# Optimization experiments

Measured on AMD Instinct MI355X. Metric: run time of the kernel, lower is better.

## Reference

```python
import jax, jax.numpy as jnp
import numpy as np

EMBED_DIM = 2048
NUM_Q_HEADS = 32
NUM_KV_HEADS = 8
HEAD_DIM = EMBED_DIM // NUM_Q_HEADS
N_REP = NUM_Q_HEADS // NUM_KV_HEADS
B, T = 2, 2048


def setup_inputs() -> dict:
    key = jax.random.key(0)
    ks = jax.random.split(key, 10)
    C = EMBED_DIM
    kv_dim = NUM_KV_HEADS * HEAD_DIM
    s = 1.0 / np.sqrt(C)
    return {
        "x": jax.random.normal(ks[0], (B, T, C), dtype=jnp.float32),
        "mask": jnp.tril(jnp.ones((1, 1, T, T), dtype=bool)),
        "Wq": jax.random.normal(ks[1], (C, C), dtype=jnp.float32) * s,
        "bq": jnp.zeros((C,), dtype=jnp.float32),
        "Wk": jax.random.normal(ks[2], (C, kv_dim), dtype=jnp.float32) * s,
        "bk": jnp.zeros((kv_dim,), dtype=jnp.float32),
        "Wv": jax.random.normal(ks[3], (C, kv_dim), dtype=jnp.float32) * s,
        "bv": jnp.zeros((kv_dim,), dtype=jnp.float32),
        "Wo": jax.random.normal(ks[4], (C, C), dtype=jnp.float32) * s,
        "bo": jnp.zeros((C,), dtype=jnp.float32),
    }


def reference(x, mask, Wq, bq, Wk, bk, Wv, bv, Wo, bo):
    b, t, c = x.shape
    # projections
    q = (x @ Wq + bq).reshape(b, t, NUM_Q_HEADS, HEAD_DIM).transpose(0, 2, 1, 3)   # [B,Hq,T,D]
    k = (x @ Wk + bk).reshape(b, t, NUM_KV_HEADS, HEAD_DIM).transpose(0, 2, 1, 3)  # [B,Hkv,T,D]
    v = (x @ Wv + bv).reshape(b, t, NUM_KV_HEADS, HEAD_DIM).transpose(0, 2, 1, 3)
    # repeat KV heads to match query heads (same math as expand+reshape)
    k = jnp.repeat(k, N_REP, axis=1)  # [B,Hq,T,D]
    v = jnp.repeat(v, N_REP, axis=1)
    scores = jnp.einsum("bhqd,bhkd->bhqk", q, k) / np.sqrt(HEAD_DIM)
    scores = jnp.where(mask, scores, -jnp.inf)
    attn = jax.nn.softmax(scores, axis=-1)
    out = jnp.einsum("bhqk,bhkd->bhqd", attn, v)  # [B,Hq,T,D]
    out = out.transpose(0, 2, 1, 3).reshape(b, t, c)
    return out @ Wo + bo
```

## Files before the change

### kernel.cpp

```cpp
#include <hip/hip_runtime.h>
#include <stdint.h>

typedef __attribute__((ext_vector_type(8))) short bf16x8;
typedef __attribute__((ext_vector_type(4))) float f32x4;

#define LOG2E 1.44269504088896f
#define T_SEQ 2048

__device__ __forceinline__ float bf2f(short s) {
    unsigned u = ((unsigned)(unsigned short)s) << 16;
    float f; __builtin_memcpy(&f, &u, 4); return f;
}
__device__ __forceinline__ short f2bf(float f) {
    unsigned u; __builtin_memcpy(&u, &f, 4);
    u = (u + 0x7FFFu + ((u >> 16) & 1u)) >> 16;
    return (short)u;
}
__device__ __forceinline__ short f2bf_trunc(float f) {
    unsigned u; __builtin_memcpy(&u, &f, 4);
    return (short)(u >> 16);
}

#define GLDS(g, l) __builtin_amdgcn_global_load_lds( \
    (const __attribute__((address_space(1))) void*)(g), \
    (__attribute__((address_space(3))) void*)(l), 16, 0, 0)

__global__ void detect_k(const unsigned short* __restrict__ x, int* __restrict__ flag) {
    int lane = threadIdx.x;
    int cnt = 0;
    for (int i = lane; i < 2048; i += 64) {
        int e = (x[i] >> 7) & 0xFF;
        if (e >= 0xC0) cnt++;
    }
    cnt += __shfl_xor(cnt, 1);
    cnt += __shfl_xor(cnt, 2);
    cnt += __shfl_xor(cnt, 4);
    cnt += __shfl_xor(cnt, 8);
    cnt += __shfl_xor(cnt, 16);
    cnt += __shfl_xor(cnt, 32);
    if (lane == 0) { flag[0] = (cnt >= 32) ? 1 : 0; flag[1] = 0; }
}

__global__ __launch_bounds__(256) void convert_k(
    const void* __restrict__ in, short* __restrict__ out, int n,
    const int* __restrict__ flag)
{
    int i = (blockIdx.x * 256 + threadIdx.x) * 8;
    if (i >= n) return;
    bf16x8 v;
    if (*flag) {
        const float* f = (const float*)in + i;
        #pragma unroll
        for (int j = 0; j < 8; ++j) v[j] = f2bf(f[j]);
    } else {
        v = *(const bf16x8*)((const short*)in + i);
    }
    *(bf16x8*)(out + i) = v;
}

__global__ __launch_bounds__(256) void convert4_k(
    const void* __restrict__ b0, const void* __restrict__ b1,
    const void* __restrict__ b2, const void* __restrict__ b3,
    short* __restrict__ o0, short* __restrict__ o1,
    short* __restrict__ o2, short* __restrict__ o3,
    const int* __restrict__ flag)
{
    int i = (blockIdx.x * 256 + threadIdx.x) * 8;
    const void* in; short* out; int off;
    if      (i < 2048) { in = b0; out = o0; off = i; }
    else if (i < 2560) { in = b1; out = o1; off = i - 2048; }
    else if (i < 3072) { in = b2; out = o2; off = i - 2560; }
    else if (i < 5120) { in = b3; out = o3; off = i - 3072; }
    else return;
    bf16x8 v;
    if (*flag) {
        const float* f = (const float*)in + off;
        #pragma unroll
        for (int j = 0; j < 8; ++j) v[j] = f2bf(f[j]);
    } else {
        v = *(const bf16x8*)((const short*)in + off);
    }
    *(bf16x8*)(out + off) = v;
}

__global__ __launch_bounds__(256) void transpose_k(
    const void* __restrict__ in_, short* __restrict__ out,
    int R, int ldi, long ibstride, long obstride, const int* __restrict__ flag)
{
    short* ob = out + (long)blockIdx.z * obstride;
    int c = blockIdx.x * 256 + threadIdx.x;
    int r0 = blockIdx.y * 64;
    int fp32 = *flag;
    if (fp32) {
        const float* ib = (const float*)in_ + (long)blockIdx.z * ibstride;
        for (int rr = 0; rr < 64; rr += 8) {
            bf16x8 v;
            #pragma unroll
            for (int j = 0; j < 8; ++j) v[j] = f2bf(ib[(long)(r0 + rr + j) * ldi + c]);
            *(bf16x8*)(ob + (long)c * R + r0 + rr) = v;
        }
    } else {
        const short* ib = (const short*)in_ + (long)blockIdx.z * ibstride;
        for (int rr = 0; rr < 64; rr += 8) {
            bf16x8 v;
            #pragma unroll
            for (int j = 0; j < 8; ++j) v[j] = ib[(long)(r0 + rr + j) * ldi + c];
            *(bf16x8*)(ob + (long)c * R + r0 + rr) = v;
        }
    }
}

#define BK 32
__global__ __launch_bounds__(256) void gemm_bt(
    const short* __restrict__ A, const short* __restrict__ Bt,
    const short* __restrict__ bias1, int nsplit,
    short* __restrict__ C, short* __restrict__ C2, int n2,
    float* __restrict__ Cf, const int* __restrict__ flag,
    int M, int N, int K, int nbx)
{
    __shared__ short a_lds[128 * BK];
    __shared__ short b_lds[128 * BK];
    const int tid = threadIdx.x;
    const int wave = tid >> 6, lane = tid & 63;
    const int quad = lane >> 4, l16 = lane & 15;

    const int nwg = gridDim.x;
    const int swz = (blockIdx.x & 7) * (nwg >> 3) + (blockIdx.x >> 3);
    const int by = swz / nbx;
    const int bx = swz - by * nbx;
    const int m0 = by * 128, n0 = bx * 128;
    const int wm = (wave >> 1) * 64, wn = (wave & 1) * 64;

    const int c0 = wave * 64 + lane;
    const int c1 = 256 + c0;
    const int row0 = c0 >> 2, kc0 = (c0 & 3) ^ ((row0 >> 1) & 3);
    const int row1 = c1 >> 2, kc1 = (c1 & 3) ^ ((row1 >> 1) & 3);
    const long aoff0 = (long)(m0 + row0) * K + kc0 * 8;
    const long aoff1 = (long)(m0 + row1) * K + kc1 * 8;
    const long boff0 = (long)(n0 + row0) * K + kc0 * 8;
    const long boff1 = (long)(n0 + row1) * K + kc1 * 8;
    short* alp0 = a_lds + (wave * 64) * 8;
    short* alp1 = a_lds + (256 + wave * 64) * 8;
    short* blp0 = b_lds + (wave * 64) * 8;
    short* blp1 = b_lds + (256 + wave * 64) * 8;

    int aro[4], bro[4];
    #pragma unroll
    for (int t = 0; t < 4; ++t) {
        int ra = wm + t * 16 + l16;
        aro[t] = ra * BK + (quad ^ ((ra >> 1) & 3)) * 8;
        int rb = wn + t * 16 + l16;
        bro[t] = rb * BK + (quad ^ ((rb >> 1) & 3)) * 8;
    }

    f32x4 acc[4][4];
    #pragma unroll
    for (int i = 0; i < 4; ++i)
        #pragma unroll
        for (int j = 0; j < 4; ++j)
            acc[i][j] = (f32x4){0.f, 0.f, 0.f, 0.f};

    for (int k0 = 0; k0 < K; k0 += BK) {
        __syncthreads();
        GLDS(A + aoff0 + k0, alp0);
        GLDS(A + aoff1 + k0, alp1);
        GLDS(Bt + boff0 + k0, blp0);
        GLDS(Bt + boff1 + k0, blp1);
        __syncthreads();
        bf16x8 af[4], bfr[4];
        #pragma unroll
        for (int t = 0; t < 4; ++t) af[t] = *(const bf16x8*)(a_lds + aro[t]);
        #pragma unroll
        for (int t = 0; t < 4; ++t) bfr[t] = *(const bf16x8*)(b_lds + bro[t]);
        #pragma unroll
        for (int mt = 0; mt < 4; ++mt)
            #pragma unroll
            for (int nt = 0; nt < 4; ++nt)
                acc[mt][nt] = __builtin_amdgcn_mfma_f32_16x16x32_bf16(
                    af[mt], bfr[nt], acc[mt][nt], 0, 0, 0);
    }

    const int f32o = Cf ? *flag : 0;
    #pragma unroll
    for (int nt = 0; nt < 4; ++nt) {
        int col = n0 + wn + nt * 16 + l16;
        float bb = bf2f(bias1[col < nsplit ? col : 0]);
        #pragma unroll
        for (int mt = 0; mt < 4; ++mt)
            #pragma unroll
            for (int r = 0; r < 4; ++r) {
                int row = m0 + wm + mt * 16 + quad * 4 + r;
                float val = acc[mt][nt][r] + bb;
                if (f32o) {
                    Cf[(long)row * N + col] = val;
                } else if (C2) {
                    if (col < n2) C[(long)row * n2 + col] = f2bf(val);
                    else          C2[(long)row * (N - n2) + (col - n2)] = f2bf(val);
                } else {
                    C[(long)row * N + col] = f2bf(val);
                }
            }
    }
}

#define PLD 68
__global__ __launch_bounds__(256, 4) void attn_k(
    const short* __restrict__ Qf, const short* __restrict__ KVf,
    const short* __restrict__ Vt, short* __restrict__ Attn)
{
    __shared__ short k_lds[64 * PLD];
    __shared__ short vt_lds[64 * PLD];
    __shared__ short p_lds[4 * 32 * PLD];
    const int tid = threadIdx.x;
    const int wave = tid >> 6, lane = tid & 63;
    const int quad = lane >> 4, l16 = lane & 15;

    const int id = blockIdx.x;
    const int bh = id & 63;
    const int w = id >> 6;
    const int QTMAP[16] = {15,13,11,9, 0,2,4,6, 14,12,10,8, 1,3,5,7};
    const int qt = QTMAP[w];
    const int b = bh >> 5, h = bh & 31, hkv = h >> 2;
    const int q0 = qt * 128;
    const int nsteps = 2 * (qt + 1);

    bf16x8 aq[2][2];
    #pragma unroll
    for (int mt = 0; mt < 2; ++mt) {
        const short* qp = Qf + ((long)(b * T_SEQ + q0 + wave * 32 + mt * 16 + l16) * 2048
                                + h * 64 + quad * 8);
        aq[mt][0] = *(const bf16x8*)qp;
        aq[mt][1] = *(const bf16x8*)(qp + 32);
        #pragma unroll
        for (int j = 0; j < 8; ++j) {
            aq[mt][0][j] = f2bf(bf2f(aq[mt][0][j]) * 0.125f);
            aq[mt][1][j] = f2bf(bf2f(aq[mt][1][j]) * 0.125f);
        }
    }

    bf16x8 onesf;
    {
        short o = (l16 == 0) ? (short)0x3F80 : (short)0;
        #pragma unroll
        for (int j = 0; j < 8; ++j) onesf[j] = o;
    }

    f32x4 o_acc[2][4];
    f32x4 l_acc[2];
    #pragma unroll
    for (int mt = 0; mt < 2; ++mt) {
        l_acc[mt] = (f32x4){0.f, 0.f, 0.f, 0.f};
        #pragma unroll
        for (int dt = 0; dt < 4; ++dt) o_acc[mt][dt] = (f32x4){0.f, 0.f, 0.f, 0.f};
    }

    const int cA = tid, cB = 256 + tid;
    const int tA = cA >> 3, chA = cA & 7;
    const int tB = cB >> 3, chB = cB & 7;
    const short* kgA = KVf + ((long)(b * T_SEQ + tA) * 1024 + hkv * 64 + chA * 8);
    const short* kgB = KVf + ((long)(b * T_SEQ + tB) * 1024 + hkv * 64 + chB * 8);
    const short* vgA = Vt + ((long)((b * 8 + hkv) * 64 + tA) * 2048 + chA * 8);
    const short* vgB = Vt + ((long)((b * 8 + hkv) * 64 + tB) * 2048 + chB * 8);

    const int rowq0 = q0 + wave * 32 + quad * 4;
    short* pw = p_lds + (wave * 32 + quad * 4) * PLD + l16;
    const short* pr = p_lds + (wave * 32 + l16) * PLD + quad * 8;

    bf16x8 kA = *(const bf16x8*)(kgA);
    bf16x8 kB = *(const bf16x8*)(kgB);
    bf16x8 vA = *(const bf16x8*)(vgA);
    bf16x8 vB = *(const bf16x8*)(vgB);

    for (int s = 0; s < nsteps; ++s) {
        const int kt0 = s * 64;
        const int ktn = ((s + 1 < nsteps) ? (s + 1) : s) * 64;
        __syncthreads();
        *(bf16x8*)(k_lds + tA * PLD + chA * 8) = kA;
        *(bf16x8*)(k_lds + tB * PLD + chB * 8) = kB;
        *(bf16x8*)(vt_lds + tA * PLD + chA * 8) = vA;
        *(bf16x8*)(vt_lds + tB * PLD + chB * 8) = vB;
        kA = *(const bf16x8*)(kgA + (long)ktn * 1024);
        kB = *(const bf16x8*)(kgB + (long)ktn * 1024);
        vA = *(const bf16x8*)(vgA + ktn);
        vB = *(const bf16x8*)(vgB + ktn);
        __syncthreads();

        const int masked = (kt0 >= q0);
        #pragma unroll
        for (int nt = 0; nt < 4; ++nt) {
            bf16x8 bk0 = *(const bf16x8*)(k_lds + (nt * 16 + l16) * PLD + quad * 8);
            bf16x8 bk1 = *(const bf16x8*)(k_lds + (nt * 16 + l16) * PLD + 32 + quad * 8);
            #pragma unroll
            for (int mt = 0; mt < 2; ++mt) {
                f32x4 z = (f32x4){0.f, 0.f, 0.f, 0.f};
                z = __builtin_amdgcn_mfma_f32_16x16x32_bf16(aq[mt][0], bk0, z, 0, 0, 0);
                z = __builtin_amdgcn_mfma_f32_16x16x32_bf16(aq[mt][1], bk1, z, 0, 0, 0);
                if (!masked) {
                    #pragma unroll
                    for (int r = 0; r < 4; ++r)
                        z[r] = exp2f(fmaf(z[r], LOG2E, -16.0f));
                } else {
                    const int rowq = rowq0 + mt * 16;
                    const int tcol = kt0 + nt * 16 + l16;
                    #pragma unroll
                    for (int r = 0; r < 4; ++r) {
                        float e = exp2f(fmaf(z[r], LOG2E, -16.0f));
                        z[r] = (tcol <= rowq + r) ? e : 0.0f;
                    }
                }
                #pragma unroll
                for (int r = 0; r < 4; ++r)
                    pw[mt * 16 * PLD + r * PLD + nt * 16] = f2bf_trunc(z[r]);
            }
        }

        bf16x8 ap[2][2];
        #pragma unroll
        for (int mt = 0; mt < 2; ++mt) {
            ap[mt][0] = *(const bf16x8*)(pr + mt * 16 * PLD);
            ap[mt][1] = *(const bf16x8*)(pr + mt * 16 * PLD + 32);
        }
        #pragma unroll
        for (int dt = 0; dt < 4; ++dt) {
            bf16x8 bv0 = *(const bf16x8*)(vt_lds + (dt * 16 + l16) * PLD + quad * 8);
            bf16x8 bv1 = *(const bf16x8*)(vt_lds + (dt * 16 + l16) * PLD + 32 + quad * 8);
            #pragma unroll
            for (int mt = 0; mt < 2; ++mt) {
                o_acc[mt][dt] = __builtin_amdgcn_mfma_f32_16x16x32_bf16(ap[mt][0], bv0, o_acc[mt][dt], 0, 0, 0);
                o_acc[mt][dt] = __builtin_amdgcn_mfma_f32_16x16x32_bf16(ap[mt][1], bv1, o_acc[mt][dt], 0, 0, 0);
            }
        }
        #pragma unroll
        for (int mt = 0; mt < 2; ++mt) {
            l_acc[mt] = __builtin_amdgcn_mfma_f32_16x16x32_bf16(ap[mt][0], onesf, l_acc[mt], 0, 0, 0);
            l_acc[mt] = __builtin_amdgcn_mfma_f32_16x16x32_bf16(ap[mt][1], onesf, l_acc[mt], 0, 0, 0);
        }
    }

    #pragma unroll
    for (int mt = 0; mt < 2; ++mt)
        #pragma unroll
        for (int r = 0; r < 4; ++r) {
            const float linv = 1.0f / __shfl(l_acc[mt][r], quad << 4);
            const int rowo = q0 + wave * 32 + mt * 16 + quad * 4 + r;
            short* ap = Attn + (long)(b * T_SEQ + rowo) * 2048 + h * 64 + l16;
            #pragma unroll
            for (int dt = 0; dt < 4; ++dt)
                ap[dt * 16] = f2bf(o_acc[mt][dt][r] * linv);
        }
}

extern "C" void kernel_launch(void* const* d_in, const int* in_sizes, int n_in,
                              void* d_out, int out_size, void* d_ws, size_t ws_size,
                              hipStream_t stream) {
    const void* x  = d_in[0];
    const void* Wq = d_in[2];
    const void* bq = d_in[3];
    const void* Wk = d_in[4];
    const void* bk = d_in[5];
    const void* Wv = d_in[6];
    const void* bv = d_in[7];
    const void* Wo = d_in[8];
    const void* bo = d_in[9];

    short* ws    = (short*)d_ws;
    int*   flags = (int*)ws;
    short* base  = ws + 16;
    short* xb    = base;
    short* Wq_t  = xb + (long)8388608;
    short* Wkv_t = Wq_t + (long)4194304;
    short* regB  = base + (long)17039360;
    short* bqb   = regB;
    short* bkb   = bqb + 2048;
    short* bvb   = bkb + 512;
    short* bob   = bvb + 512;
    short* Wo_t  = bob + 2048;
    short* Qf    = Wo_t + (long)4194304;
    short* KVf   = Qf + (long)8388608;
    short* Vtp   = KVf + (long)4194304;
    short* Attn  = Vtp + (long)2097152;

    detect_k<<<1, 64, 0, stream>>>((const unsigned short*)x, flags);

    convert_k<<<4096, 256, 0, stream>>>(x, xb, 4096 * 2048, flags);
    convert4_k<<<3, 256, 0, stream>>>(bq, bk, bv, bo, bqb, bkb, bvb, bob, flags);

    transpose_k<<<dim3(8, 32, 1), 256, 0, stream>>>(Wq, Wq_t, 2048, 2048, 0L, 0L, flags);
    transpose_k<<<dim3(2, 32, 1), 256, 0, stream>>>(Wk, Wkv_t, 2048, 512, 0L, 0L, flags);
    transpose_k<<<dim3(2, 32, 1), 256, 0, stream>>>(Wv, Wkv_t + (long)512 * 2048, 2048, 512, 0L, 0L, flags);
    transpose_k<<<dim3(8, 32, 1), 256, 0, stream>>>(Wo, Wo_t, 2048, 2048, 0L, 0L, flags);

    gemm_bt<<<768, 256, 0, stream>>>(xb, Wq_t, bqb, 3072,
                                     Qf, KVf, 2048, nullptr, flags,
                                     4096, 3072, 2048, 24);

    transpose_k<<<dim3(2, 32, 2), 256, 0, stream>>>(KVf + 512, Vtp, 2048, 1024,
                                                    (long)2048 * 1024, (long)512 * 2048, flags + 1);

    attn_k<<<1024, 256, 0, stream>>>(Qf, KVf, Vtp, Attn);

    gemm_bt<<<512, 256, 0, stream>>>(Attn, Wo_t, bob, 2048,
                                     (short*)d_out, nullptr, 0,
                                     (float*)d_out, flags,
                                     4096, 2048, 2048, 16);
}
```

Before: 450.9 us.

## Fuse conversion and transpose launches, shrink GEMM N-tiles to fill more CUs

Merges the x/bias conversion kernels into one launch and the four weight transposes into one launch, which cuts launch overhead. Templates the GEMM on the N-tile width so the QKV projection uses 128x96 tiles and the output projection uses 128x64 tiles. Both GEMMs now launch 1024 workgroups instead of 768/512, which should fill the 256 CUs more evenly. The cost is less operand reuse per tile and partially idle waves during B-tile loads.

```diff
diff --git a/kernel.cpp b/kernel.cpp
--- a/kernel.cpp
+++ b/kernel.cpp
@@ -41,31 +41,30 @@
     if (lane == 0) { flag[0] = (cnt >= 32) ? 1 : 0; flag[1] = 0; }
 }
 
-__global__ __launch_bounds__(256) void convert_k(
-    const void* __restrict__ in, short* __restrict__ out, int n,
-    const int* __restrict__ flag)
-{
-    int i = (blockIdx.x * 256 + threadIdx.x) * 8;
-    if (i >= n) return;
-    bf16x8 v;
-    if (*flag) {
-        const float* f = (const float*)in + i;
-        #pragma unroll
-        for (int j = 0; j < 8; ++j) v[j] = f2bf(f[j]);
-    } else {
-        v = *(const bf16x8*)((const short*)in + i);
-    }
-    *(bf16x8*)(out + i) = v;
-}
-
-__global__ __launch_bounds__(256) void convert4_k(
+__global__ __launch_bounds__(256) void convert_all_k(
+    const void* __restrict__ x, short* __restrict__ xb,
     const void* __restrict__ b0, const void* __restrict__ b1,
     const void* __restrict__ b2, const void* __restrict__ b3,
     short* __restrict__ o0, short* __restrict__ o1,
     short* __restrict__ o2, short* __restrict__ o3,
     const int* __restrict__ flag)
 {
-    int i = (blockIdx.x * 256 + threadIdx.x) * 8;
+    const int blk = blockIdx.x;
+    const int fp32 = *flag;
+    if (blk < 4096) {
+        int i = (blk * 256 + threadIdx.x) * 8;
+        bf16x8 v;
+        if (fp32) {
+            const float* f = (const float*)x + i;
+            #pragma unroll
+            for (int j = 0; j < 8; ++j) v[j] = f2bf(f[j]);
+        } else {
+            v = *(const bf16x8*)((const short*)x + i);
+        }
+        *(bf16x8*)(xb + i) = v;
+        return;
+    }
+    int i = ((blk - 4096) * 256 + threadIdx.x) * 8;
     const void* in; short* out; int off;
     if      (i < 2048) { in = b0; out = o0; off = i; }
     else if (i < 2560) { in = b1; out = o1; off = i - 2048; }
@@ -73,7 +72,7 @@
     else if (i < 5120) { in = b3; out = o3; off = i - 3072; }
     else return;
     bf16x8 v;
-    if (*flag) {
+    if (fp32) {
         const float* f = (const float*)in + off;
         #pragma unroll
         for (int j = 0; j < 8; ++j) v[j] = f2bf(f[j]);
@@ -110,7 +109,41 @@
     }
 }
 
+__global__ __launch_bounds__(256) void transpose4_k(
+    const void* __restrict__ Wq, const void* __restrict__ Wk,
+    const void* __restrict__ Wv, const void* __restrict__ Wo,
+    short* __restrict__ Wq_t, short* __restrict__ Wkv_t,
+    short* __restrict__ Wo_t, const int* __restrict__ flag)
+{
+    const int bx = blockIdx.x;
+    const void* in; short* out; int ldi, c;
+    if (bx < 8)       { in = Wq; out = Wq_t;                     ldi = 2048; c = bx * 256 + threadIdx.x; }
+    else if (bx < 10) { in = Wk; out = Wkv_t;                    ldi = 512;  c = (bx - 8) * 256 + threadIdx.x; }
+    else if (bx < 12) { in = Wv; out = Wkv_t + (long)512 * 2048; ldi = 512;  c = (bx - 10) * 256 + threadIdx.x; }
+    else              { in = Wo; out = Wo_t;                     ldi = 2048; c = (bx - 12) * 256 + threadIdx.x; }
+    const int r0 = blockIdx.y * 64;
+    const int fp32 = *flag;
+    if (fp32) {
+        const float* ib = (const float*)in;
+        for (int rr = 0; rr < 64; rr += 8) {
+            bf16x8 v;
+            #pragma unroll
+            for (int j = 0; j < 8; ++j) v[j] = f2bf(ib[(long)(r0 + rr + j) * ldi + c]);
+            *(bf16x8*)(out + (long)c * 2048 + r0 + rr) = v;
+        }
+    } else {
+        const short* ib = (const short*)in;
+        for (int rr = 0; rr < 64; rr += 8) {
+            bf16x8 v;
+            #pragma unroll
+            for (int j = 0; j < 8; ++j) v[j] = ib[(long)(r0 + rr + j) * ldi + c];
+            *(bf16x8*)(out + (long)c * 2048 + r0 + rr) = v;
+        }
+    }
+}
+
 #define BK 32
+template <int BN>
 __global__ __launch_bounds__(256) void gemm_bt(
     const short* __restrict__ A, const short* __restrict__ Bt,
     const short* __restrict__ bias1, int nsplit,
@@ -118,8 +151,9 @@
     float* __restrict__ Cf, const int* __restrict__ flag,
     int M, int N, int K, int nbx)
 {
+    constexpr int NT = BN / 32;
     __shared__ short a_lds[128 * BK];
-    __shared__ short b_lds[128 * BK];
+    __shared__ short b_lds[BN * BK];
     const int tid = threadIdx.x;
     const int wave = tid >> 6, lane = tid & 63;
     const int quad = lane >> 4, l16 = lane & 15;
@@ -128,36 +162,38 @@
     const int swz = (blockIdx.x & 7) * (nwg >> 3) + (blockIdx.x >> 3);
     const int by = swz / nbx;
     const int bx = swz - by * nbx;
-    const int m0 = by * 128, n0 = bx * 128;
-    const int wm = (wave >> 1) * 64, wn = (wave & 1) * 64;
-
-    const int c0 = wave * 64 + lane;
-    const int c1 = 256 + c0;
-    const int row0 = c0 >> 2, kc0 = (c0 & 3) ^ ((row0 >> 1) & 3);
-    const int row1 = c1 >> 2, kc1 = (c1 & 3) ^ ((row1 >> 1) & 3);
-    const long aoff0 = (long)(m0 + row0) * K + kc0 * 8;
-    const long aoff1 = (long)(m0 + row1) * K + kc1 * 8;
-    const long boff0 = (long)(n0 + row0) * K + kc0 * 8;
-    const long boff1 = (long)(n0 + row1) * K + kc1 * 8;
+    const int m0 = by * 128, n0 = bx * BN;
+    const int wm = (wave >> 1) * 64, wn = (wave & 1) * (BN / 2);
+
+    const int c0i = tid, c1i = 256 + tid;
+    const int rA0 = c0i >> 2, kc0 = (c0i & 3) ^ ((rA0 >> 1) & 3);
+    const int rA1 = c1i >> 2, kc1 = (c1i & 3) ^ ((rA1 >> 1) & 3);
+    const long aoff0 = (long)(m0 + rA0) * K + kc0 * 8;
+    const long aoff1 = (long)(m0 + rA1) * K + kc1 * 8;
+    const long boff0 = (long)(n0 + rA0) * K + kc0 * 8;
+    const long boff1 = (long)(n0 + rA1) * K + kc1 * 8;
     short* alp0 = a_lds + (wave * 64) * 8;
     short* alp1 = a_lds + (256 + wave * 64) * 8;
     short* blp0 = b_lds + (wave * 64) * 8;
     short* blp1 = b_lds + (256 + wave * 64) * 8;
 
-    int aro[4], bro[4];
+    int aro[4], bro[NT];
     #pragma unroll
     for (int t = 0; t < 4; ++t) {
         int ra = wm + t * 16 + l16;
         aro[t] = ra * BK + (quad ^ ((ra >> 1) & 3)) * 8;
+    }
+    #pragma unroll
+    for (int t = 0; t < NT; ++t) {
         int rb = wn + t * 16 + l16;
         bro[t] = rb * BK + (quad ^ ((rb >> 1) & 3)) * 8;
     }
 
-    f32x4 acc[4][4];
+    f32x4 acc[4][NT];
     #pragma unroll
     for (int i = 0; i < 4; ++i)
         #pragma unroll
-        for (int j = 0; j < 4; ++j)
+        for (int j = 0; j < NT; ++j)
             acc[i][j] = (f32x4){0.f, 0.f, 0.f, 0.f};
 
     for (int k0 = 0; k0 < K; k0 += BK) {
@@ -165,24 +201,28 @@
         GLDS(A + aoff0 + k0, alp0);
         GLDS(A + aoff1 + k0, alp1);
         GLDS(Bt + boff0 + k0, blp0);
-        GLDS(Bt + boff1 + k0, blp1);
+        if constexpr (BN == 128) {
+            GLDS(Bt + boff1 + k0, blp1);
+        } else if constexpr (BN == 96) {
+            if (wave < 2) GLDS(Bt + boff1 + k0, blp1);
+        }
         __syncthreads();
-        bf16x8 af[4], bfr[4];
+        bf16x8 af[4], bfr[NT];
         #pragma unroll
         for (int t = 0; t < 4; ++t) af[t] = *(const bf16x8*)(a_lds + aro[t]);
         #pragma unroll
-        for (int t = 0; t < 4; ++t) bfr[t] = *(const bf16x8*)(b_lds + bro[t]);
+        for (int t = 0; t < NT; ++t) bfr[t] = *(const bf16x8*)(b_lds + bro[t]);
         #pragma unroll
         for (int mt = 0; mt < 4; ++mt)
             #pragma unroll
-            for (int nt = 0; nt < 4; ++nt)
+            for (int nt = 0; nt < NT; ++nt)
                 acc[mt][nt] = __builtin_amdgcn_mfma_f32_16x16x32_bf16(
                     af[mt], bfr[nt], acc[mt][nt], 0, 0, 0);
     }
 
     const int f32o = Cf ? *flag : 0;
     #pragma unroll
-    for (int nt = 0; nt < 4; ++nt) {
+    for (int nt = 0; nt < NT; ++nt) {
         int col = n0 + wn + nt * 16 + l16;
         float bb = bf2f(bias1[col < nsplit ? col : 0]);
         #pragma unroll
@@ -382,25 +422,23 @@
 
     detect_k<<<1, 64, 0, stream>>>((const unsigned short*)x, flags);
 
-    convert_k<<<4096, 256, 0, stream>>>(x, xb, 4096 * 2048, flags);
-    convert4_k<<<3, 256, 0, stream>>>(bq, bk, bv, bo, bqb, bkb, bvb, bob, flags);
-
-    transpose_k<<<dim3(8, 32, 1), 256, 0, stream>>>(Wq, Wq_t, 2048, 2048, 0L, 0L, flags);
-    transpose_k<<<dim3(2, 32, 1), 256, 0, stream>>>(Wk, Wkv_t, 2048, 512, 0L, 0L, flags);
-    transpose_k<<<dim3(2, 32, 1), 256, 0, stream>>>(Wv, Wkv_t + (long)512 * 2048, 2048, 512, 0L, 0L, flags);
-    transpose_k<<<dim3(8, 32, 1), 256, 0, stream>>>(Wo, Wo_t, 2048, 2048, 0L, 0L, flags);
-
-    gemm_bt<<<768, 256, 0, stream>>>(xb, Wq_t, bqb, 3072,
-                                     Qf, KVf, 2048, nullptr, flags,
-                                     4096, 3072, 2048, 24);
+    convert_all_k<<<4099, 256, 0, stream>>>(x, xb, bq, bk, bv, bo,
+                                            bqb, bkb, bvb, bob, flags);
+
+    transpose4_k<<<dim3(20, 32), 256, 0, stream>>>(Wq, Wk, Wv, Wo,
+                                                   Wq_t, Wkv_t, Wo_t, flags);
+
+    gemm_bt<96><<<1024, 256, 0, stream>>>(xb, Wq_t, bqb, 3072,
+                                          Qf, KVf, 2048, nullptr, flags,
+                                          4096, 3072, 2048, 32);
 
     transpose_k<<<dim3(2, 32, 2), 256, 0, stream>>>(KVf + 512, Vtp, 2048, 1024,
                                                     (long)2048 * 1024, (long)512 * 2048, flags + 1);
 
     attn_k<<<1024, 256, 0, stream>>>(Qf, KVf, Vtp, Attn);
 
-    gemm_bt<<<512, 256, 0, stream>>>(Attn, Wo_t, bob, 2048,
-                                     (short*)d_out, nullptr, 0,
-                                     (float*)d_out, flags,
-                                     4096, 2048, 2048, 16);
-}
+    gemm_bt<64><<<1024, 256, 0, stream>>>(Attn, Wo_t, bob, 2048,
+                                          (short*)d_out, nullptr, 0,
+                                          (float*)d_out, flags,
+                                          4096, 2048, 2048, 32);
+}
```

After: 462.1 us. 2.5% more time.
